# Performance work log

Measured on AMD Instinct MI355X. Metric: run time of the kernel, lower is better.

## Reference

```python
import jax, jax.numpy as jnp
import numpy as np

# hyper_params (mode='test')
PRE_NMS = 1000
POST_NMS = 300
IOU_TH = 0.7
VARIANCES = np.array([0.1, 0.1, 0.2, 0.2], dtype=np.float32)
FM = 64            # feature map height/width
ANCHOR_COUNT = 9   # 3 scales x 3 ratios


def _make_anchors():
    """Normalized [y1,x1,y2,x2] anchors on a FM x FM grid, 9 per cell."""
    scales = np.array([0.1, 0.2, 0.4], np.float32)
    ratios = np.array([0.5, 1.0, 2.0], np.float32)
    ws = (scales[:, None] * np.sqrt(ratios)[None, :]).reshape(-1)  # (9,)
    hs = (scales[:, None] / np.sqrt(ratios)[None, :]).reshape(-1)  # (9,)
    ctr = (np.arange(FM, dtype=np.float32) + 0.5) / FM
    cy, cx = np.meshgrid(ctr, ctr, indexing='ij')                  # (FM,FM)
    cy = cy[..., None]; cx = cx[..., None]                         # (FM,FM,1)
    anchors = np.stack([cy - 0.5 * hs, cx - 0.5 * ws,
                        cy + 0.5 * hs, cx + 0.5 * ws], axis=-1)    # (FM,FM,9,4)
    return jnp.asarray(anchors.reshape(-1, 4))                     # (36864,4)


def setup_inputs() -> dict:
    key = jax.random.key(0)
    k1, k2 = jax.random.split(key)
    B = 16
    rpn_bbox_deltas = jax.random.normal(k1, (B, FM, FM, ANCHOR_COUNT * 4), dtype=jnp.float32)
    rpn_labels = jax.random.uniform(k2, (B, FM, FM, ANCHOR_COUNT), dtype=jnp.float32)
    return {"rpn_bbox_deltas": rpn_bbox_deltas,
            "rpn_labels": rpn_labels,
            "anchors": _make_anchors()}


def _nms_single(boxes):
    """Greedy NMS on score-sorted boxes (N,4) -> (POST_NMS,4), zero-padded."""
    N = boxes.shape[0]
    y1, x1, y2, x2 = boxes[:, 0], boxes[:, 1], boxes[:, 2], boxes[:, 3]
    area = (y2 - y1) * (x2 - x1)                                   # (N,)
    iy1 = jnp.maximum(y1[:, None], y1[None, :])
    ix1 = jnp.maximum(x1[:, None], x1[None, :])
    iy2 = jnp.minimum(y2[:, None], y2[None, :])
    ix2 = jnp.minimum(x2[:, None], x2[None, :])
    inter = jnp.maximum(iy2 - iy1, 0.0) * jnp.maximum(ix2 - ix1, 0.0)
    iou = inter / jnp.maximum(area[:, None] + area[None, :] - inter, 1e-9)  # (N,N)
    idx = jnp.arange(N)

    def body(i, keep):
        # if box i survives, suppress later boxes with high overlap
        suppress = keep[i] & (iou[i] > IOU_TH) & (idx > i)
        return keep & ~suppress

    keep = jax.lax.fori_loop(0, N, body, jnp.ones((N,), dtype=bool))
    # stable sort: kept boxes first, original (score-descending) order preserved
    order = jnp.argsort(jnp.where(keep, 0, 1))[:POST_NMS]
    sel = boxes[order]
    valid = keep[order]
    # combined_non_max_suppression clips output boxes to [0,1] and zero-pads
    return jnp.where(valid[:, None], jnp.clip(sel, 0.0, 1.0), 0.0)


def reference(rpn_bbox_deltas, rpn_labels, anchors):
    B = rpn_bbox_deltas.shape[0]
    N = anchors.shape[0]
    deltas = rpn_bbox_deltas.reshape(B, N, 4) * jnp.asarray(VARIANCES)
    labels = rpn_labels.reshape(B, N)

    # decode deltas against anchors
    anc_h = anchors[:, 2] - anchors[:, 0]
    anc_w = anchors[:, 3] - anchors[:, 1]
    anc_cy = anchors[:, 0] + 0.5 * anc_h
    anc_cx = anchors[:, 1] + 0.5 * anc_w
    h = jnp.exp(deltas[..., 2]) * anc_h
    w = jnp.exp(deltas[..., 3]) * anc_w
    cy = deltas[..., 0] * anc_h + anc_cy
    cx = deltas[..., 1] * anc_w + anc_cx
    boxes = jnp.stack([cy - 0.5 * h, cx - 0.5 * w,
                       cy + 0.5 * h, cx + 0.5 * w], axis=-1)       # (B,N,4)

    # top-k by objectness score (descending, so NMS input is pre-sorted)
    _, pre_idx = jax.lax.top_k(labels, PRE_NMS)                    # (B,PRE_NMS)
    pre_boxes = jnp.take_along_axis(boxes, pre_idx[..., None], axis=1)  # (B,PRE_NMS,4)

    roi_bboxes = jax.vmap(_nms_single)(pre_boxes)                  # (B,POST_NMS,4)
    return jax.lax.stop_gradient(roi_bboxes)
```

## Files before the change

### kernel.cpp

```cpp
#include <hip/hip_runtime.h>
#include <stdint.h>

#pragma clang fp contract(off)

#define N_ANCH 36864
#define PRE_NMS 1000
#define POST_NMS 300
#define SEL_CAP 1024
#define NWAVE 16

#define SLICES 16
#define K1_NT 256
#define SLICE_KEYS 2304
#define KEYS_PT 9
#define SLICE_TOP 128
#define COMPACT_CAP 192
#define MERGE_CAP 2048

#define NCOPY 8
#define HSTR 257

#define M_WSTRIDE 1024
#define M_WORDS_PER_B 16384
#define WS_BOX_FLOATS_PER_B 5120

#define K3_NT 512

__device__ __forceinline__ uint32_t mono_key(float v) {
    uint32_t u = __float_as_uint(v);
    return (u & 0x80000000u) ? ~u : (u | 0x80000000u);
}

__device__ __forceinline__ float clip01(float x) {
    return fminf(fmaxf(x, 0.0f), 1.0f);
}

__device__ __forceinline__ uint64_t bcast64(uint64_t v, int srclane) {
    uint32_t lo = (uint32_t)v, hi = (uint32_t)(v >> 32);
    lo = __builtin_amdgcn_readlane(lo, srclane);
    hi = __builtin_amdgcn_readlane(hi, srclane);
    return ((uint64_t)hi << 32) | (uint64_t)lo;
}

__device__ __forceinline__ uint64_t sfl64(uint64_t v) {
    uint32_t lo = __builtin_amdgcn_readfirstlane((uint32_t)v);
    uint32_t hi = __builtin_amdgcn_readfirstlane((uint32_t)(v >> 32));
    return ((uint64_t)hi << 32) | (uint64_t)lo;
}

__device__ __forceinline__ uint64_t bfly_or64(uint64_t v) {
    v |= __shfl_xor(v, 32);
    v |= __shfl_xor(v, 16);
    v |= __shfl_xor(v, 8);
    v |= __shfl_xor(v, 4);
    v |= __shfl_xor(v, 2);
    v |= __shfl_xor(v, 1);
    return v;
}

__device__ __forceinline__ void scan256(const uint32_t* __restrict__ h, uint32_t K,
                                        uint32_t* shm, uint32_t& outBin, uint32_t& outKrem) {
    const int t    = threadIdx.x;
    const int lane = t & 63;
    const int wv   = t >> 6;
    const uint32_t q = h[t];
    uint32_t sfx = q, o;
    o = __shfl_down(sfx, 1);  if (lane < 63) sfx += o;
    o = __shfl_down(sfx, 2);  if (lane < 62) sfx += o;
    o = __shfl_down(sfx, 4);  if (lane < 60) sfx += o;
    o = __shfl_down(sfx, 8);  if (lane < 56) sfx += o;
    o = __shfl_down(sfx, 16); if (lane < 48) sfx += o;
    o = __shfl_down(sfx, 32); if (lane < 32) sfx += o;
    if (lane == 0) shm[wv] = sfx;
    __syncthreads();
    uint32_t wAbove = 0;
    for (int w2 = wv + 1; w2 < 4; ++w2) wAbove += shm[w2];
    const uint32_t above = wAbove + (sfx - q);
    if ((above < K) && (above + q >= K)) { shm[4] = (uint32_t)t; shm[5] = K - above; }
    __syncthreads();
    outBin  = shm[4];
    outKrem = shm[5];
}

__global__ __launch_bounds__(K1_NT) void k1s_slice_top(
    const float* __restrict__ labels,
    uint64_t* __restrict__ wsCand)
{
    const int s = blockIdx.x;
    const int b = blockIdx.y;
    const int t = threadIdx.x;
    const int lane = t & 63;

    __shared__ uint32_t hc[NCOPY * HSTR];
    __shared__ uint32_t red[256];
    __shared__ uint32_t red2[256];
    __shared__ uint32_t shm[8];
    __shared__ uint64_t cand[COMPACT_CAP];
    __shared__ uint32_t scnt;

    const float* lab = labels + (size_t)b * N_ANCH + (size_t)s * SLICE_KEYS;
    uint32_t key[KEYS_PT];
#pragma unroll
    for (int r = 0; r < KEYS_PT; ++r)
        key[r] = mono_key(lab[r * K1_NT + t]);

    for (int i = t; i < NCOPY * HSTR; i += K1_NT) hc[i] = 0u;
    red2[t] = 0u;
    if (t == 0) scnt = 0u;
    __syncthreads();

    const int cbase = (lane & 7) * HSTR;
#pragma unroll
    for (int r = 0; r < KEYS_PT; ++r)
        atomicAdd(&hc[cbase + (key[r] >> 24)], 1u);
    __syncthreads();
    uint32_t sum = 0;
#pragma unroll
    for (int c = 0; c < NCOPY; ++c) sum += hc[c * HSTR + t];
    red[t] = sum;
    uint32_t b0, krem;
    scan256(red, SLICE_TOP, shm, b0, krem);

#pragma unroll
    for (int r = 0; r < KEYS_PT; ++r)
        if ((key[r] >> 24) == b0) atomicAdd(&red2[(key[r] >> 16) & 0xFFu], 1u);
    __syncthreads();
    uint32_t b1, krem2;
    scan256(red2, krem, shm, b1, krem2);
    const uint32_t thresh16 = (b0 << 8) | b1;

#pragma unroll
    for (int r = 0; r < KEYS_PT; ++r) {
        const uint32_t u = key[r];
        const bool pred = (u >> 16) >= thresh16;
        const uint64_t bal = __ballot(pred ? 1 : 0);
        uint32_t base = 0;
        if (lane == 0 && bal)
            base = atomicAdd(&scnt, (uint32_t)__popcll(bal));
        base = __shfl(base, 0);
        if (pred) {
            const uint32_t off = (uint32_t)__popcll(bal & ((1ull << lane) - 1ull));
            const uint32_t pos = base + off;
            const uint32_t gi = (uint32_t)(s * SLICE_KEYS + r * K1_NT + t);
            if (pos < COMPACT_CAP)
                cand[pos] = ((uint64_t)u << 32) | (uint64_t)(0xFFFFFFFFu - gi);
        }
    }
    __syncthreads();
    uint32_t c = scnt; if (c > COMPACT_CAP) c = COMPACT_CAP;
    if (t >= (int)c && t < COMPACT_CAP) cand[t] = 0ull;
    __syncthreads();

    if (t < COMPACT_CAP) {
        const uint64_t mine = cand[t];
        uint32_t rank = 0;
        for (int i = 0; i < COMPACT_CAP; i += 4)
            rank += (cand[i]     > mine) + (cand[i + 1] > mine)
                  + (cand[i + 2] > mine) + (cand[i + 3] > mine);
        if (t < (int)c && rank < SLICE_TOP)
            wsCand[((size_t)b * SLICES + s) * SLICE_TOP + rank] = mine;
    }
}

__global__ __launch_bounds__(K1_NT) void k1m_merge_decode(
    const float* __restrict__ deltas,
    const float* __restrict__ anchors,
    const uint64_t* __restrict__ wsCand,
    float* __restrict__ wsBox)
{
    const int chunk = blockIdx.x;
    const int b     = blockIdx.y;
    const int t     = threadIdx.x;

    __shared__ __align__(16) uint64_t keyA[MERGE_CAP];
    const uint4* c4 = (const uint4*)(wsCand + (size_t)b * MERGE_CAP);
    uint4* k4 = (uint4*)keyA;
#pragma unroll
    for (int i = t; i < MERGE_CAP / 2; i += K1_NT) k4[i] = c4[i];
    __syncthreads();

    if (t < SLICE_TOP) {
        const uint64_t mine = keyA[chunk * SLICE_TOP + t];
        uint32_t lo[SLICES];
#pragma unroll
        for (int r = 0; r < SLICES; ++r) lo[r] = 0u;

#pragma unroll
        for (uint32_t s2 = 128; s2 > 0; s2 >>= 1) {
            uint64_t probe[SLICES];
#pragma unroll
            for (int r = 0; r < SLICES; ++r) {
                const uint32_t idx = lo[r] + s2 - 1u;
                probe[r] = keyA[r * SLICE_TOP + (idx < 128u ? idx : 0u)];
            }
#pragma unroll
            for (int r = 0; r < SLICES; ++r) {
                const uint32_t idx = lo[r] + s2 - 1u;
                if (idx < 128u && probe[r] > mine) lo[r] += s2;
            }
        }
        uint32_t rank = 0;
#pragma unroll
        for (int r = 0; r < SLICES; ++r) rank += lo[r];

        if (rank < PRE_NMS) {
            uint32_t idx = 0xFFFFFFFFu - (uint32_t)(mine & 0xFFFFFFFFull);
            float4 d4 = *(const float4*)(deltas + ((size_t)b * N_ANCH + idx) * 4);
            float4 a4 = *(const float4*)(anchors + (size_t)idx * 4);
            float anc_h  = a4.z - a4.x;
            float anc_w  = a4.w - a4.y;
            float anc_cy = a4.x + 0.5f * anc_h;
            float anc_cx = a4.y + 0.5f * anc_w;
            float dy = d4.x * 0.1f, dx = d4.y * 0.1f;
            float dh = d4.z * 0.2f, dw = d4.w * 0.2f;
            float h  = expf(dh) * anc_h;
            float w  = expf(dw) * anc_w;
            float cy = dy * anc_h + anc_cy;
            float cx = dx * anc_w + anc_cx;
            float y1 = cy - 0.5f * h, x1 = cx - 0.5f * w;
            float y2 = cy + 0.5f * h, x2 = cx + 0.5f * w;
            float* wb = wsBox + (size_t)b * WS_BOX_FLOATS_PER_B;
            wb[rank]              = y1;
            wb[SEL_CAP + rank]    = x1;
            wb[2*SEL_CAP + rank]  = y2;
            wb[3*SEL_CAP + rank]  = x2;
            wb[4*SEL_CAP + rank]  = (y2 - y1) * (x2 - x1);
        }
    }
}

__global__ __launch_bounds__(1024) void k2_iou_matrix(
    const float* __restrict__ wsBox,
    uint64_t* __restrict__ wsM)
{
    const int gx   = blockIdx.x;
    const int b    = blockIdx.y;
    const int t    = threadIdx.x;
    const int lane = t & 63;
    const int wave = t >> 6;

    int cb, r0, r1;
    if (gx < 16) { cb = gx;     r0 = 0;   r1 = 64 * (cb + 1); if (r1 > 512) r1 = 512; }
    else         { cb = gx - 8; r0 = 512; r1 = 64 * (cb + 1); }
    if (r1 > PRE_NMS) r1 = PRE_NMS;

    __shared__ float s[5 * SEL_CAP];
    const float4* b4 = (const float4*)(wsBox + (size_t)b * WS_BOX_FLOATS_PER_B);
    float4* s4 = (float4*)s;
    for (int i = t; i < (5 * SEL_CAP) / 4; i += 1024) s4[i] = b4[i];
    __syncthreads();

    float* ly1 = s;
    float* lx1 = s + SEL_CAP;
    float* ly2 = s + 2 * SEL_CAP;
    float* lx2 = s + 3 * SEL_CAP;
    float* lar = s + 4 * SEL_CAP;

    const int j = cb * 64 + lane;
    const float y1j = ly1[j], x1j = lx1[j], y2j = ly2[j], x2j = lx2[j], aj = lar[j];

    uint64_t* Mb = wsM + (size_t)b * M_WORDS_PER_B + (size_t)cb * M_WSTRIDE;
    for (int i = r0 + wave; i < r1; i += NWAVE) {
        float iy1 = fmaxf(ly1[i], y1j);
        float ix1 = fmaxf(lx1[i], x1j);
        float iy2 = fminf(ly2[i], y2j);
        float ix2 = fminf(lx2[i], x2j);
        float ih = iy2 - iy1; if (ih < 0.f) ih = 0.f;
        float iw = ix2 - ix1; if (iw < 0.f) iw = 0.f;
        float inter = ih * iw;
        float denom = lar[i] + aj - inter;
        if (denom < 1e-9f) denom = 1e-9f;
        float iou = inter / denom;
        bool sup = (j > i) && (iou > 0.7f);
        uint64_t mask = __ballot(sup ? 1 : 0);
        if (lane == 0) Mb[i] = mask;
    }
}

__global__ __launch_bounds__(K3_NT) void k3_reduce_out(
    const float* __restrict__ wsBox,
    const uint64_t* __restrict__ wsM,
    float* __restrict__ out)
{
    const int b    = blockIdx.x;
    const int t    = threadIdx.x;
    const int lane = t & 63;
    const int wave = t >> 6;

    __shared__ uint64_t remv[16];
    __shared__ uint64_t keepW[16];
    __shared__ uint32_t wordPref[16];

    const uint64_t* Mg = wsM + (size_t)b * M_WORDS_PER_B;

    if (t < 16) remv[t] = 0ull;

    uint64_t dA = 0, dB = 0, sAB = 0, brA2 = 0, brB2 = 0, brA3 = 0, brB3 = 0;
    uint64_t mA1 = 0, mB1 = 0, mA2 = 0, mB2 = 0;
    if (wave == 0) {
        dA   = Mg[lane];
        dB   = Mg[(size_t)1 * M_WSTRIDE + 64 + lane];
        sAB  = Mg[(size_t)1 * M_WSTRIDE + lane];
        brA2 = Mg[(size_t)2 * M_WSTRIDE + lane];
        brB2 = Mg[(size_t)2 * M_WSTRIDE + 64 + lane];
        brA3 = Mg[(size_t)3 * M_WSTRIDE + lane];
        brB3 = Mg[(size_t)3 * M_WSTRIDE + 64 + lane];
    } else if (wave <= 6) {
        const int v1 = 2 * wave + 2, v2 = 2 * wave + 3;
        mA1 = Mg[(size_t)v1 * M_WSTRIDE + lane];
        mB1 = Mg[(size_t)v1 * M_WSTRIDE + 64 + lane];
        mA2 = Mg[(size_t)v2 * M_WSTRIDE + lane];
        mB2 = Mg[(size_t)v2 * M_WSTRIDE + 64 + lane];
    }
    uint64_t bridgeA = 0ull, bridgeB = 0ull;
    __syncthreads();

    for (int p = 0; p < 8; ++p) {
        if (wave == 0) {
            const int a = 2 * p, bw = 2 * p + 1;
            const uint64_t mda = dA, mdb = dB, msab = sAB;
            const uint64_t b2a = brA2, b2b = brB2, b3a = brA3, b3b = brB3;
            if (p < 7) {
                const int an = 2 * p + 2, bn = 2 * p + 3;
                dA  = Mg[(size_t)an * M_WSTRIDE + 64 * an + lane];
                dB  = Mg[(size_t)bn * M_WSTRIDE + 64 * bn + lane];
                sAB = Mg[(size_t)bn * M_WSTRIDE + 64 * an + lane];
                if (p < 6) {
                    const int a3 = 2 * p + 4, b3 = 2 * p + 5;
                    brA2 = Mg[(size_t)a3 * M_WSTRIDE + 64 * an + lane];
                    brB2 = Mg[(size_t)a3 * M_WSTRIDE + 64 * bn + lane];
                    brA3 = Mg[(size_t)b3 * M_WSTRIDE + 64 * an + lane];
                    brB3 = Mg[(size_t)b3 * M_WSTRIDE + 64 * bn + lane];
                }
            }
            uint64_t curA = sfl64(remv[a]) | sfl64(bridgeA);
            {
                const uint64_t amS = sfl64(bfly_or64(mda));
                const uint64_t Q        = amS & ~curA;
                const uint64_t keptSure = ~curA & ~Q;
                curA |= sfl64(bfly_or64(((keptSure >> lane) & 1ull) ? mda : 0ull));
                uint64_t work = Q & ~curA;
                while (work) {
                    const int bp = (int)__builtin_ctzll(work);
                    curA |= bcast64(mda, bp);
                    work &= ~(1ull << bp);
                    work &= ~curA;
                }
            }
            const uint64_t keepA = ~curA;
            const uint64_t sc = bfly_or64(((keepA >> lane) & 1ull) ? msab : 0ull);
            const uint64_t validB = (bw == 15) ? ((1ull << 40) - 1ull) : ~0ull;
            uint64_t curB = sfl64(remv[bw]) | sfl64(bridgeB) | sfl64(sc);
            {
                const bool lv = (bw < 15) || (lane < 40);
                const uint64_t amS = sfl64(bfly_or64(lv ? mdb : 0ull));
                const uint64_t Q        = amS & ~curB & validB;
                const uint64_t keptSure = validB & ~curB & ~Q;
                curB |= sfl64(bfly_or64(((keptSure >> lane) & 1ull) ? mdb : 0ull));
                uint64_t work = Q & ~curB;
                while (work) {
                    const int bp = (int)__builtin_ctzll(work);
                    curB |= bcast64(mdb, bp);
                    work &= ~(1ull << bp);
                    work &= ~curB;
                }
            }
            const uint64_t keepB = (~curB) & validB;
            if (lane == 0) { keepW[a] = keepA; keepW[bw] = keepB; }
            if (p < 7) {
                bridgeA = bfly_or64((((keepA >> lane) & 1ull) ? b2a : 0ull) |
                                    (((keepB >> lane) & 1ull) ? b2b : 0ull));
                bridgeB = bfly_or64((((keepA >> lane) & 1ull) ? b3a : 0ull) |
                                    (((keepB >> lane) & 1ull) ? b3b : 0ull));
            }
        } else if (wave <= 6 && p >= 1 && p <= wave) {
            const int v1 = 2 * wave + 2, v2 = 2 * wave + 3;
            const uint64_t a1 = mA1, b1 = mB1, a2 = mA2, b2 = mB2;
            if (p < wave) {
                mA1 = Mg[(size_t)v1 * M_WSTRIDE + 64 * (2 * p)     + lane];
                mB1 = Mg[(size_t)v1 * M_WSTRIDE + 64 * (2 * p + 1) + lane];
                mA2 = Mg[(size_t)v2 * M_WSTRIDE + 64 * (2 * p)     + lane];
                mB2 = Mg[(size_t)v2 * M_WSTRIDE + 64 * (2 * p + 1) + lane];
            }
            const uint64_t kmA = keepW[2 * p - 2];
            const uint64_t kmB = keepW[2 * p - 1];
            uint64_t x1 = (((kmA >> lane) & 1ull) ? a1 : 0ull) |
                          (((kmB >> lane) & 1ull) ? b1 : 0ull);
            x1 = bfly_or64(x1);
            uint64_t x2 = (((kmA >> lane) & 1ull) ? a2 : 0ull) |
                          (((kmB >> lane) & 1ull) ? b2 : 0ull);
            x2 = bfly_or64(x2);
            if (lane == 0) { remv[v1] |= x1; remv[v2] |= x2; }
        }
        __syncthreads();
    }

    if (t == 0) {
        uint32_t acc = 0u;
        for (int w = 0; w < 16; ++w) {
            wordPref[w] = acc;
            acc += (uint32_t)__popcll(keepW[w]);
        }
    }
    float* ob = out + (size_t)b * (POST_NMS * 4);
    for (int i = t; i < POST_NMS * 4; i += K3_NT) ob[i] = 0.0f;
    __syncthreads();

    for (int tt = t; tt < PRE_NMS; tt += K3_NT) {
        const int w = tt >> 6, bpos = tt & 63;
        uint64_t kw = keepW[w];
        if ((kw >> bpos) & 1ull) {
            uint32_t rank = wordPref[w] +
                            (uint32_t)__popcll(kw & ((1ull << bpos) - 1ull));
            if (rank < POST_NMS) {
                const float* wb = wsBox + (size_t)b * WS_BOX_FLOATS_PER_B;
                float* o = ob + (size_t)rank * 4;
                o[0] = clip01(wb[tt]);
                o[1] = clip01(wb[SEL_CAP + tt]);
                o[2] = clip01(wb[2*SEL_CAP + tt]);
                o[3] = clip01(wb[3*SEL_CAP + tt]);
            }
        }
    }
}

extern "C" void kernel_launch(void* const* d_in, const int* in_sizes, int n_in,
                              void* d_out, int out_size, void* d_ws, size_t ws_size,
                              hipStream_t stream) {
    const float* deltas  = (const float*)d_in[0];
    const float* labels  = (const float*)d_in[1];
    const float* anchors = (const float*)d_in[2];
    float* out = (float*)d_out;
    const int B = in_sizes[1] / N_ANCH;

    char* p = (char*)d_ws;
    uint64_t* wsCand = (uint64_t*)p;
    float*    wsBox  = (float*)(p + (size_t)B * MERGE_CAP * 8);
    uint64_t* wsM    = (uint64_t*)(p + (size_t)B * MERGE_CAP * 8
                                     + (size_t)B * WS_BOX_FLOATS_PER_B * 4);

    k1s_slice_top<<<dim3(SLICES, B), K1_NT, 0, stream>>>(labels, wsCand);
    k1m_merge_decode<<<dim3(SLICES, B), K1_NT, 0, stream>>>(deltas, anchors, wsCand, wsBox);
    k2_iou_matrix<<<dim3(24, B), 1024, 0, stream>>>(wsBox, wsM);
    k3_reduce_out<<<B, K3_NT, 0, stream>>>(wsBox, wsM, out);
}
```

Before: 106.7 us.

## Use fixed-threshold fast path in slice top-k and split merge ranking across thread pairs

The slice top-k kernel first compacts candidates against a fixed score threshold picked for the expected score distribution. It runs the two-pass radix histogram only when the candidate count falls outside [128, 256], and the compaction buffer grows to 256 entries. The merge/decode kernel now assigns two threads per candidate, each binary-searching 8 of the 16 slices, and combines the partial ranks with a shuffle. The aim is to skip the histogram, atomics and barriers in the common case and to halve serial search depth. The cost is a data-dependent fast path, a larger rank-counting loop, and redundant work when the fallback fires.

```diff
diff --git a/kernel.cpp b/kernel.cpp
--- a/kernel.cpp
+++ b/kernel.cpp
@@ -14,7 +14,7 @@
 #define SLICE_KEYS 2304
 #define KEYS_PT 9
 #define SLICE_TOP 128
-#define COMPACT_CAP 192
+#define CAP2 256
 #define MERGE_CAP 2048
 
 #define NCOPY 8
@@ -95,7 +95,7 @@
     __shared__ uint32_t red[256];
     __shared__ uint32_t red2[256];
     __shared__ uint32_t shm[8];
-    __shared__ uint64_t cand[COMPACT_CAP];
+    __shared__ uint64_t cand[CAP2];
     __shared__ uint32_t scnt;
 
     const float* lab = labels + (size_t)b * N_ANCH + (size_t)s * SLICE_KEYS;
@@ -109,30 +109,11 @@
     if (t == 0) scnt = 0u;
     __syncthreads();
 
-    const int cbase = (lane & 7) * HSTR;
-#pragma unroll
-    for (int r = 0; r < KEYS_PT; ++r)
-        atomicAdd(&hc[cbase + (key[r] >> 24)], 1u);
-    __syncthreads();
-    uint32_t sum = 0;
-#pragma unroll
-    for (int c = 0; c < NCOPY; ++c) sum += hc[c * HSTR + t];
-    red[t] = sum;
-    uint32_t b0, krem;
-    scan256(red, SLICE_TOP, shm, b0, krem);
-
-#pragma unroll
-    for (int r = 0; r < KEYS_PT; ++r)
-        if ((key[r] >> 24) == b0) atomicAdd(&red2[(key[r] >> 16) & 0xFFu], 1u);
-    __syncthreads();
-    uint32_t b1, krem2;
-    scan256(red2, krem, shm, b1, krem2);
-    const uint32_t thresh16 = (b0 << 8) | b1;
-
+    const uint32_t KTAU = mono_key(0.91666667f);
 #pragma unroll
     for (int r = 0; r < KEYS_PT; ++r) {
         const uint32_t u = key[r];
-        const bool pred = (u >> 16) >= thresh16;
+        const bool pred = (u >= KTAU);
         const uint64_t bal = __ballot(pred ? 1 : 0);
         uint32_t base = 0;
         if (lane == 0 && bal)
@@ -142,24 +123,64 @@
             const uint32_t off = (uint32_t)__popcll(bal & ((1ull << lane) - 1ull));
             const uint32_t pos = base + off;
             const uint32_t gi = (uint32_t)(s * SLICE_KEYS + r * K1_NT + t);
-            if (pos < COMPACT_CAP)
+            if (pos < CAP2)
                 cand[pos] = ((uint64_t)u << 32) | (uint64_t)(0xFFFFFFFFu - gi);
         }
     }
     __syncthreads();
-    uint32_t c = scnt; if (c > COMPACT_CAP) c = COMPACT_CAP;
-    if (t >= (int)c && t < COMPACT_CAP) cand[t] = 0ull;
-    __syncthreads();
-
-    if (t < COMPACT_CAP) {
-        const uint64_t mine = cand[t];
-        uint32_t rank = 0;
-        for (int i = 0; i < COMPACT_CAP; i += 4)
-            rank += (cand[i]     > mine) + (cand[i + 1] > mine)
-                  + (cand[i + 2] > mine) + (cand[i + 3] > mine);
-        if (t < (int)c && rank < SLICE_TOP)
-            wsCand[((size_t)b * SLICES + s) * SLICE_TOP + rank] = mine;
-    }
+    uint32_t c = scnt;
+
+    if (c < SLICE_TOP || c > CAP2) {
+        if (t == 0) scnt = 0u;
+        const int cbase = (lane & 7) * HSTR;
+#pragma unroll
+        for (int r = 0; r < KEYS_PT; ++r)
+            atomicAdd(&hc[cbase + (key[r] >> 24)], 1u);
+        __syncthreads();
+        uint32_t sum = 0;
+#pragma unroll
+        for (int cc = 0; cc < NCOPY; ++cc) sum += hc[cc * HSTR + t];
+        red[t] = sum;
+        uint32_t b0, krem;
+        scan256(red, SLICE_TOP, shm, b0, krem);
+#pragma unroll
+        for (int r = 0; r < KEYS_PT; ++r)
+            if ((key[r] >> 24) == b0) atomicAdd(&red2[(key[r] >> 16) & 0xFFu], 1u);
+        __syncthreads();
+        uint32_t b1, krem2;
+        scan256(red2, krem, shm, b1, krem2);
+        const uint32_t thresh16 = (b0 << 8) | b1;
+#pragma unroll
+        for (int r = 0; r < KEYS_PT; ++r) {
+            const uint32_t u = key[r];
+            const bool pred = (u >> 16) >= thresh16;
+            const uint64_t bal = __ballot(pred ? 1 : 0);
+            uint32_t base = 0;
+            if (lane == 0 && bal)
+                base = atomicAdd(&scnt, (uint32_t)__popcll(bal));
+            base = __shfl(base, 0);
+            if (pred) {
+                const uint32_t off = (uint32_t)__popcll(bal & ((1ull << lane) - 1ull));
+                const uint32_t pos = base + off;
+                const uint32_t gi = (uint32_t)(s * SLICE_KEYS + r * K1_NT + t);
+                if (pos < CAP2)
+                    cand[pos] = ((uint64_t)u << 32) | (uint64_t)(0xFFFFFFFFu - gi);
+            }
+        }
+        __syncthreads();
+        c = scnt; if (c > CAP2) c = CAP2;
+    }
+
+    if (t >= (int)c) cand[t] = 0ull;
+    __syncthreads();
+
+    const uint64_t mine = cand[t];
+    uint32_t rank = 0;
+    for (int i = 0; i < CAP2; i += 4)
+        rank += (cand[i]     > mine) + (cand[i + 1] > mine)
+              + (cand[i + 2] > mine) + (cand[i + 3] > mine);
+    if (t < (int)c && rank < SLICE_TOP)
+        wsCand[((size_t)b * SLICES + s) * SLICE_TOP + rank] = mine;
 }
 
 __global__ __launch_bounds__(K1_NT) void k1m_merge_decode(
@@ -179,53 +200,55 @@
     for (int i = t; i < MERGE_CAP / 2; i += K1_NT) k4[i] = c4[i];
     __syncthreads();
 
-    if (t < SLICE_TOP) {
-        const uint64_t mine = keyA[chunk * SLICE_TOP + t];
-        uint32_t lo[SLICES];
-#pragma unroll
-        for (int r = 0; r < SLICES; ++r) lo[r] = 0u;
-
-#pragma unroll
-        for (uint32_t s2 = 128; s2 > 0; s2 >>= 1) {
-            uint64_t probe[SLICES];
-#pragma unroll
-            for (int r = 0; r < SLICES; ++r) {
-                const uint32_t idx = lo[r] + s2 - 1u;
-                probe[r] = keyA[r * SLICE_TOP + (idx < 128u ? idx : 0u)];
-            }
-#pragma unroll
-            for (int r = 0; r < SLICES; ++r) {
-                const uint32_t idx = lo[r] + s2 - 1u;
-                if (idx < 128u && probe[r] > mine) lo[r] += s2;
-            }
-        }
-        uint32_t rank = 0;
-#pragma unroll
-        for (int r = 0; r < SLICES; ++r) rank += lo[r];
-
-        if (rank < PRE_NMS) {
-            uint32_t idx = 0xFFFFFFFFu - (uint32_t)(mine & 0xFFFFFFFFull);
-            float4 d4 = *(const float4*)(deltas + ((size_t)b * N_ANCH + idx) * 4);
-            float4 a4 = *(const float4*)(anchors + (size_t)idx * 4);
-            float anc_h  = a4.z - a4.x;
-            float anc_w  = a4.w - a4.y;
-            float anc_cy = a4.x + 0.5f * anc_h;
-            float anc_cx = a4.y + 0.5f * anc_w;
-            float dy = d4.x * 0.1f, dx = d4.y * 0.1f;
-            float dh = d4.z * 0.2f, dw = d4.w * 0.2f;
-            float h  = expf(dh) * anc_h;
-            float w  = expf(dw) * anc_w;
-            float cy = dy * anc_h + anc_cy;
-            float cx = dx * anc_w + anc_cx;
-            float y1 = cy - 0.5f * h, x1 = cx - 0.5f * w;
-            float y2 = cy + 0.5f * h, x2 = cx + 0.5f * w;
-            float* wb = wsBox + (size_t)b * WS_BOX_FLOATS_PER_B;
-            wb[rank]              = y1;
-            wb[SEL_CAP + rank]    = x1;
-            wb[2*SEL_CAP + rank]  = y2;
-            wb[3*SEL_CAP + rank]  = x2;
-            wb[4*SEL_CAP + rank]  = (y2 - y1) * (x2 - x1);
-        }
+    const int p    = t >> 1;
+    const int half = t & 1;
+    const uint64_t mine = keyA[chunk * SLICE_TOP + p];
+    uint32_t lo[8];
+#pragma unroll
+    for (int r = 0; r < 8; ++r) lo[r] = 0u;
+    const int rbase = half * 8;
+
+#pragma unroll
+    for (uint32_t s2 = 128; s2 > 0; s2 >>= 1) {
+        uint64_t probe[8];
+#pragma unroll
+        for (int r = 0; r < 8; ++r) {
+            const uint32_t idx = lo[r] + s2 - 1u;
+            probe[r] = keyA[(rbase + r) * SLICE_TOP + (idx < 128u ? idx : 0u)];
+        }
+#pragma unroll
+        for (int r = 0; r < 8; ++r) {
+            const uint32_t idx = lo[r] + s2 - 1u;
+            if (idx < 128u && probe[r] > mine) lo[r] += s2;
+        }
+    }
+    uint32_t rank8 = 0;
+#pragma unroll
+    for (int r = 0; r < 8; ++r) rank8 += lo[r];
+    const uint32_t rank = rank8 + __shfl_xor(rank8, 1);
+
+    if (half == 0 && rank < PRE_NMS) {
+        uint32_t idx = 0xFFFFFFFFu - (uint32_t)(mine & 0xFFFFFFFFull);
+        float4 d4 = *(const float4*)(deltas + ((size_t)b * N_ANCH + idx) * 4);
+        float4 a4 = *(const float4*)(anchors + (size_t)idx * 4);
+        float anc_h  = a4.z - a4.x;
+        float anc_w  = a4.w - a4.y;
+        float anc_cy = a4.x + 0.5f * anc_h;
+        float anc_cx = a4.y + 0.5f * anc_w;
+        float dy = d4.x * 0.1f, dx = d4.y * 0.1f;
+        float dh = d4.z * 0.2f, dw = d4.w * 0.2f;
+        float h  = expf(dh) * anc_h;
+        float w  = expf(dw) * anc_w;
+        float cy = dy * anc_h + anc_cy;
+        float cx = dx * anc_w + anc_cx;
+        float y1 = cy - 0.5f * h, x1 = cx - 0.5f * w;
+        float y2 = cy + 0.5f * h, x2 = cx + 0.5f * w;
+        float* wb = wsBox + (size_t)b * WS_BOX_FLOATS_PER_B;
+        wb[rank]              = y1;
+        wb[SEL_CAP + rank]    = x1;
+        wb[2*SEL_CAP + rank]  = y2;
+        wb[3*SEL_CAP + rank]  = x2;
+        wb[4*SEL_CAP + rank]  = (y2 - y1) * (x2 - x1);
     }
 }
 
```

Result: no change. 105.4 us (median of 2 runs) (-1.2%).
